# Performance work log

Hardware: AMD Instinct MI355X
Metric: run time of the kernel (lower is better)

The kernel has to match this reference:

```python
import jax, jax.numpy as jnp
import numpy as np

S, I = 512, 384
C_MSA, C_Z, H, C = 64, 128, 8, 32
EPS = 1e-5


def _layernorm(x, g, b):
    mu = jnp.mean(x, axis=-1, keepdims=True)
    var = jnp.var(x, axis=-1, keepdims=True)
    return (x - mu) * jax.lax.rsqrt(var + EPS) * g + b


def setup_inputs() -> dict:
    key = jax.random.key(0)
    ks = jax.random.split(key, 6)
    sc_v = 1.0 / np.sqrt(C_MSA)
    sc_z = 1.0 / np.sqrt(C_Z)
    sc_o = 1.0 / np.sqrt(H * C)
    return {
        "msa_SI": jax.random.normal(ks[0], (S, I, C_MSA), jnp.float32),
        "pair_II": jax.random.normal(ks[1], (I, I, C_Z), jnp.float32),
        "ln_msa_g": jnp.ones((C_MSA,), jnp.float32),
        "ln_msa_b": jnp.zeros((C_MSA,), jnp.float32),
        "ln_pair_g": jnp.ones((C_Z,), jnp.float32),
        "ln_pair_b": jnp.zeros((C_Z,), jnp.float32),
        "W_v": jax.random.normal(ks[2], (C_MSA, H * C), jnp.float32) * sc_v,
        "W_bias": jax.random.normal(ks[3], (C_Z, H), jnp.float32) * sc_z,
        "W_gate": jax.random.normal(ks[4], (C_MSA, H * C), jnp.float32) * sc_v,
        "W_out": jax.random.normal(ks[5], (H * C, C_MSA), jnp.float32) * sc_o,
    }


def reference(msa_SI, pair_II, ln_msa_g, ln_msa_b, ln_pair_g, ln_pair_b,
              W_v, W_bias, W_gate, W_out):
    s, i = msa_SI.shape[:2]
    msa_n = _layernorm(msa_SI, ln_msa_g, ln_msa_b)              # [S,I,Cm]
    v_SIHC = (msa_n @ W_v).reshape(s, i, H, C)                   # [S,I,H,C]
    bias_IIH = _layernorm(pair_II, ln_pair_g, ln_pair_b) @ W_bias  # [I,I,H]
    w_IIH = jax.nn.softmax(bias_IIH, axis=-2)                    # softmax over j
    gate = jax.nn.sigmoid(msa_n @ W_gate)                        # [S,I,H*C]
    # weighted average shared across S: [I,I,H] x [S,I,H,C] -> [S,I,H,C]
    weights = jnp.einsum('ijh,sjhc->sihc', w_IIH, v_SIHC).reshape(s, i, H * C)
    o = gate * weights
    return o @ W_out                                             # [S,I,Cm]
```

## Files before the change

### kernel.cpp

```cpp
#include <hip/hip_runtime.h>
#include <hip/hip_bf16.h>

#define S_DIM 512
#define I_DIM 384
#define CM 64
#define CZ 128
#define H_DIM 8
#define C_DIM 32
#define HC 256
#define II (I_DIM*I_DIM)

typedef short bf16x8 __attribute__((ext_vector_type(8)));
typedef float f32x4 __attribute__((ext_vector_type(4)));

__device__ __forceinline__ float s2f(short s) {
    unsigned int u = ((unsigned int)(unsigned short)s) << 16;
    float f; __builtin_memcpy(&f, &u, 4); return f;
}
__device__ __forceinline__ short f2bf(float f) {
    __hip_bfloat16 h = __float2bfloat16(f);
    short r; __builtin_memcpy(&r, &h, 2); return r;
}

__device__ __forceinline__ void glds16(const short* g, short* l) {
    __builtin_amdgcn_global_load_lds(
        (const __attribute__((address_space(1))) void*)g,
        (__attribute__((address_space(3))) void*)l, 16, 0, 0);
}

__global__ __launch_bounds__(256) void k_pair_ln_bias(
    const float* __restrict__ pair, const float* __restrict__ g,
    const float* __restrict__ b, const float* __restrict__ Wb,
    float* __restrict__ bias)
{
    __shared__ float xs[4][CZ];
    __shared__ float WbT[H_DIM*132];
    const int tid = threadIdx.x;
    const int wv = tid >> 6, lane = tid & 63;
    const int ij = blockIdx.x*4 + wv;

    {
        float4 q = *(const float4*)(Wb + tid*4);
        int m = tid*4;
        WbT[(m&7)*132 + (m>>3)]     = q.x;
        WbT[((m+1)&7)*132 + ((m+1)>>3)] = q.y;
        WbT[((m+2)&7)*132 + ((m+2)>>3)] = q.z;
        WbT[((m+3)&7)*132 + ((m+3)>>3)] = q.w;
    }

    float2 x2 = *(const float2*)(pair + (size_t)ij*CZ + lane*2);
    float s1 = x2.x + x2.y;
    float s2 = x2.x*x2.x + x2.y*x2.y;
#pragma unroll
    for (int off = 32; off > 0; off >>= 1) {
        s1 += __shfl_xor(s1, off, 64);
        s2 += __shfl_xor(s2, off, 64);
    }
    float mu = s1 * (1.f/CZ);
    float var = s2 * (1.f/CZ) - mu*mu;
    float rs = rsqrtf(var + 1e-5f);
    xs[wv][lane*2]   = (x2.x - mu)*rs*g[lane*2]   + b[lane*2];
    xs[wv][lane*2+1] = (x2.y - mu)*rs*g[lane*2+1] + b[lane*2+1];
    __syncthreads();

    const int h = lane >> 3, seg = lane & 7;
    float p = 0.f;
#pragma unroll
    for (int jj = 0; jj < 16; jj++) {
        int c = seg + jj*8;
        p += xs[wv][c] * WbT[h*132 + c];
    }
    p += __shfl_down(p, 4, 64);
    p += __shfl_down(p, 2, 64);
    p += __shfl_down(p, 1, 64);
    if (seg == 0) bias[(size_t)h*II + ij] = p;
}

__global__ __launch_bounds__(384) void k_softmax(
    const float* __restrict__ bias, short* __restrict__ w)
{
    int blk = blockIdx.x;
    int i = blk >> 3, h = blk & 7;
    int j = threadIdx.x;
    float x = bias[(size_t)h*II + i*I_DIM + j];
    float m = x;
#pragma unroll
    for (int off = 32; off > 0; off >>= 1) m = fmaxf(m, __shfl_xor(m, off, 64));
    __shared__ float red[6];
    int wv = j >> 6;
    if ((j & 63) == 0) red[wv] = m;
    __syncthreads();
    m = red[0];
#pragma unroll
    for (int k = 1; k < 6; k++) m = fmaxf(m, red[k]);
    float e = __expf(x - m);
    float s = e;
#pragma unroll
    for (int off = 32; off > 0; off >>= 1) s += __shfl_xor(s, off, 64);
    __syncthreads();
    if ((j & 63) == 0) red[wv] = s;
    __syncthreads();
    s = 0.f;
#pragma unroll
    for (int k = 0; k < 6; k++) s += red[k];
    w[(size_t)h*II + i*I_DIM + j] = f2bf(e / s);
}

__global__ __launch_bounds__(256) void k_prep_w(
    const float* __restrict__ Wv, const float* __restrict__ Wg,
    const float* __restrict__ Wo,
    short* __restrict__ Wt, short* __restrict__ Wot)
{
    int idx = blockIdx.x*256 + threadIdx.x;
    if (idx < 512*64) {
        int n = idx >> 6, k = idx & 63;
        Wt[idx] = f2bf((n < HC) ? Wv[k*HC + n] : Wg[k*HC + (n - HC)]);
    } else {
        int q = idx - 512*64;
        int n = q >> 8, k = q & 255;
        Wot[q] = f2bf(Wo[k*64 + n]);
    }
}

__global__ __launch_bounds__(256) void k4_ln_vgate(
    const float* __restrict__ msa_c,
    const float* __restrict__ gm, const float* __restrict__ bm,
    const short* __restrict__ Wt,
    short* __restrict__ v_t, short* __restrict__ gate)
{
    __shared__ alignas(16) short lds[20992];
    short* As = lds;
    short* Bs = lds + 4608;
    short* T  = lds;

    const int tid = threadIdx.x;
    const int wave = tid >> 6;
    const int lane = tid & 63;
    const int pm = blockIdx.y;

    {
        const int row = tid >> 2;
        const int seg = tid & 3;
        float xf[16], gf[16], bf[16];
        const float* rp = msa_c + (size_t)(pm*64 + row)*CM + seg*16;
#pragma unroll
        for (int q = 0; q < 4; q++) {
            float4 a = *(const float4*)(rp + q*4);
            xf[q*4] = a.x; xf[q*4+1] = a.y; xf[q*4+2] = a.z; xf[q*4+3] = a.w;
            float4 gg = *(const float4*)(gm + seg*16 + q*4);
            gf[q*4] = gg.x; gf[q*4+1] = gg.y; gf[q*4+2] = gg.z; gf[q*4+3] = gg.w;
            float4 bb = *(const float4*)(bm + seg*16 + q*4);
            bf[q*4] = bb.x; bf[q*4+1] = bb.y; bf[q*4+2] = bb.z; bf[q*4+3] = bb.w;
        }
        float s1 = 0.f, s2 = 0.f;
#pragma unroll
        for (int j = 0; j < 16; j++) { s1 += xf[j]; s2 += xf[j]*xf[j]; }
        s1 += __shfl_xor(s1, 1); s2 += __shfl_xor(s2, 1);
        s1 += __shfl_xor(s1, 2); s2 += __shfl_xor(s2, 2);
        float mu = s1 * (1.f/64.f);
        float var = s2 * (1.f/64.f) - mu*mu;
        float rs = rsqrtf(var + 1e-5f);
        bf16x8 o0, o1;
#pragma unroll
        for (int j = 0; j < 8; j++) {
            o0[j] = f2bf((xf[j]   - mu)*rs*gf[j]   + bf[j]);
            o1[j] = f2bf((xf[8+j] - mu)*rs*gf[8+j] + bf[8+j]);
        }
        *(bf16x8*)&As[row*72 + seg*16]     = o0;
        *(bf16x8*)&As[row*72 + seg*16 + 8] = o1;
    }

    const int lr = lane >> 2, lq = lane & 3;
    const int fr = lane & 15, fq = lane >> 4;
    f32x4 acc[4][8] = {};

    for (int kt = 0; kt < 2; ++kt) {
#pragma unroll
        for (int c2 = 0; c2 < 8; c2++) {
            int ch = wave + c2*4;
            glds16(Wt + (ch*16 + lr)*64 + kt*32 + lq*8, &Bs[ch*512]);
        }
        __syncthreads();

        bf16x8 af[4], bfrag[8];
#pragma unroll
        for (int mi = 0; mi < 4; mi++)
            af[mi] = *(const bf16x8*)&As[(mi*16 + fr)*72 + kt*32 + fq*8];
#pragma unroll
        for (int ni = 0; ni < 8; ni++)
            bfrag[ni] = *(const bf16x8*)&Bs[(wave*128 + ni*16 + fr)*32 + fq*8];
#pragma unroll
        for (int mi = 0; mi < 4; mi++)
#pragma unroll
            for (int ni = 0; ni < 8; ni++)
                acc[mi][ni] = __builtin_amdgcn_mfma_f32_16x16x32_bf16(
                    af[mi], bfrag[ni], acc[mi][ni], 0, 0, 0);
        __syncthreads();
    }

    const int s_local = pm / 6;
    const int j0 = (pm % 6) * 64;
    if (wave < 2) {
#pragma unroll
        for (int mi = 0; mi < 4; mi++)
#pragma unroll
        for (int ni = 0; ni < 8; ni++) {
            int cl = wave*128 + ni*16 + fr;
            short4 pk;
            pk.x = f2bf(acc[mi][ni][0]);
            pk.y = f2bf(acc[mi][ni][1]);
            pk.z = f2bf(acc[mi][ni][2]);
            pk.w = f2bf(acc[mi][ni][3]);
            *(short4*)&T[cl*72 + mi*16 + fq*4] = pk;
        }
    } else {
#pragma unroll
        for (int mi = 0; mi < 4; mi++)
#pragma unroll
        for (int ni = 0; ni < 8; ni++)
#pragma unroll
        for (int r = 0; r < 4; r++) {
            int rowg = pm*64 + mi*16 + fq*4 + r;
            int col = (wave - 2)*128 + ni*16 + fr;
            gate[(size_t)rowg*HC + col] =
                f2bf(1.f/(1.f + __expf(-acc[mi][ni][r])));
        }
    }
    __syncthreads();
#pragma unroll
    for (int p = 0; p < 8; p++) {
        int unit = p*256 + tid;
        int cl = unit >> 3, part = unit & 7;
        bf16x8 d = *(const bf16x8*)&T[cl*72 + part*8];
        int h = cl >> 5, cc = cl & 31;
        *(bf16x8*)&v_t[(((size_t)s_local*H_DIM + h)*C_DIM + cc)*I_DIM + j0 + part*8] = d;
    }
}

__global__ __launch_bounds__(512, 2) void k56_einsum_proj(
    const short* __restrict__ w,
    const short* __restrict__ v_t,
    const short* __restrict__ gate,
    const short* __restrict__ Wot,
    float* __restrict__ out)
{
    __shared__ alignas(16) short Ws[3][192*32];
    __shared__ alignas(16) short Ob[8][32*40];
    const int tid = threadIdx.x;
    const int wave = tid >> 6, lane = tid & 63;
    const int fr = lane & 15, fq = lane >> 4;
    const int ibase = blockIdx.x * 192;
    const int sg = blockIdx.y;
    const int ms = wave >> 1;
    const int kv = wave & 1;
    const int s  = sg*4 + ms;
    const int iw = kv * 96;

    const short* vts = v_t + (size_t)s * H_DIM * C_DIM * I_DIM;

    auto stage = [&](int h_, int kt_, int buf) {
        const short* base = w + (size_t)h_*II + (size_t)kt_*32;
        {
            int row = wave*16 + (lane >> 2);
            int q = (lane & 3) ^ ((row >> 1) & 3);
            glds16(base + (size_t)(ibase + row)*I_DIM + q*8,
                   &Ws[buf][wave*16*32]);
        }
        if (wave < 4) {
            int row = (8 + wave)*16 + (lane >> 2);
            int q = (lane & 3) ^ ((row >> 1) & 3);
            glds16(base + (size_t)(ibase + row)*I_DIM + q*8,
                   &Ws[buf][(8 + wave)*16*32]);
        }
    };
    auto loadAv = [&](bf16x8* d, int h_, int kt_) {
        const short* vb = vts + (size_t)h_*(C_DIM*I_DIM) + kt_*32;
        d[0] = *(const bf16x8*)&vb[fr*I_DIM + fq*8];
        d[1] = *(const bf16x8*)&vb[(16 + fr)*I_DIM + fq*8];
    };

    f32x4 acc_o[6][4] = {};
    bf16x8 avs[3][2];

    loadAv(avs[0], 0, 0);
    loadAv(avs[1], 0, 1);
    __builtin_amdgcn_sched_barrier(0);
    stage(0, 0, 0);
    stage(0, 1, 1);
    stage(0, 2, 2);
    __builtin_amdgcn_sched_barrier(0);

#pragma unroll 1
    for (int h = 0; h < H_DIM; h++) {
        f32x4 acc_e[2][6] = {};
#pragma unroll
        for (int kt = 0; kt < 12; kt++) {
            const int cb = kt % 3;
            if (h == 0 && kt == 0) {
                if (wave < 4) asm volatile("s_waitcnt vmcnt(4)" ::: "memory");
                else          asm volatile("s_waitcnt vmcnt(2)" ::: "memory");
            } else if (h == 7 && kt == 10) {
                if (wave < 4) asm volatile("s_waitcnt vmcnt(4)" ::: "memory");
                else          asm volatile("s_waitcnt vmcnt(3)" ::: "memory");
            } else if (h == 7 && kt == 11) {
                asm volatile("s_waitcnt vmcnt(0)" ::: "memory");
            } else {
                if (wave < 4) asm volatile("s_waitcnt vmcnt(6)" ::: "memory");
                else          asm volatile("s_waitcnt vmcnt(4)" ::: "memory");
            }
            __builtin_amdgcn_s_barrier();
            __builtin_amdgcn_sched_barrier(0);

            bf16x8 bwv[6];
#pragma unroll
            for (int ni = 0; ni < 6; ni++) {
                int row = iw + ni*16 + fr;
                bwv[ni] = *(const bf16x8*)
                    &Ws[cb][row*32 + ((fq ^ ((row >> 1) & 3)) << 3)];
            }
            if (kt < 10)      loadAv(avs[(kt+2)%3], h, kt + 2);
            else if (h < 7)   loadAv(avs[(kt+2)%3], h + 1, kt - 10);
            __builtin_amdgcn_sched_barrier(0);

            asm volatile("s_waitcnt lgkmcnt(0)" ::: "memory");
            __builtin_amdgcn_sched_barrier(0);
            __builtin_amdgcn_s_barrier();
            __builtin_amdgcn_sched_barrier(0);

            if (kt < 9)       stage(h, kt + 3, cb);
            else if (h < 7)   stage(h + 1, kt - 9, cb);
            __builtin_amdgcn_sched_barrier(0);

            __builtin_amdgcn_s_setprio(1);
#pragma unroll
            for (int mi = 0; mi < 2; mi++)
#pragma unroll
                for (int ni = 0; ni < 6; ni++)
                    acc_e[mi][ni] = __builtin_amdgcn_mfma_f32_16x16x32_bf16(
                        avs[cb][mi], bwv[ni], acc_e[mi][ni], 0, 0, 0);
            __builtin_amdgcn_s_setprio(0);
        }

        bf16x8 bw[4];
#pragma unroll
        for (int ni = 0; ni < 4; ni++)
            bw[ni] = *(const bf16x8*)&Wot[(ni*16 + fr)*HC + h*C_DIM + fq*8];
        short4 gv[2][6];
#pragma unroll
        for (int mi = 0; mi < 2; mi++)
#pragma unroll
        for (int ni = 0; ni < 6; ni++)
            gv[mi][ni] = *(const short4*)&gate[
                (size_t)(s*I_DIM + ibase + iw + ni*16 + fr)*HC
                + h*C_DIM + mi*16 + fq*4];

        short* myOb = Ob[wave];
#pragma unroll
        for (int p = 0; p < 3; p++) {
#pragma unroll
            for (int t = 0; t < 2; t++) {
                int ni = p*2 + t;
#pragma unroll
                for (int mi = 0; mi < 2; mi++) {
                    short4 g = gv[mi][ni];
                    short4 pk;
                    pk.x = f2bf(acc_e[mi][ni][0] * s2f(g.x));
                    pk.y = f2bf(acc_e[mi][ni][1] * s2f(g.y));
                    pk.z = f2bf(acc_e[mi][ni][2] * s2f(g.z));
                    pk.w = f2bf(acc_e[mi][ni][3] * s2f(g.w));
                    *(short4*)&myOb[(t*16 + fr)*40 + mi*16 + fq*4] = pk;
                }
            }
            bf16x8 ao[2];
#pragma unroll
            for (int t = 0; t < 2; t++)
                ao[t] = *(const bf16x8*)&myOb[(t*16 + fr)*40 + fq*8];
            __builtin_amdgcn_s_setprio(1);
#pragma unroll
            for (int t = 0; t < 2; t++)
#pragma unroll
                for (int ni = 0; ni < 4; ni++)
                    acc_o[p*2 + t][ni] = __builtin_amdgcn_mfma_f32_16x16x32_bf16(
                        ao[t], bw[ni], acc_o[p*2 + t][ni], 0, 0, 0);
            __builtin_amdgcn_s_setprio(0);
        }
    }

#pragma unroll
    for (int mi = 0; mi < 6; mi++)
#pragma unroll
    for (int ni = 0; ni < 4; ni++)
#pragma unroll
    for (int r = 0; r < 4; r++) {
        int i = ibase + iw + mi*16 + fq*4 + r;
        int n = ni*16 + fr;
        out[(size_t)(s*I_DIM + i)*CM + n] = acc_o[mi][ni][r];
    }
}

extern "C" void kernel_launch(void* const* d_in, const int* in_sizes, int n_in,
                              void* d_out, int out_size, void* d_ws, size_t ws_size,
                              hipStream_t stream)
{
    const float* msa  = (const float*)d_in[0];
    const float* pair = (const float*)d_in[1];
    const float* gm   = (const float*)d_in[2];
    const float* bm   = (const float*)d_in[3];
    const float* gp   = (const float*)d_in[4];
    const float* bp   = (const float*)d_in[5];
    const float* Wv   = (const float*)d_in[6];
    const float* Wb   = (const float*)d_in[7];
    const float* Wg   = (const float*)d_in[8];
    const float* Wo   = (const float*)d_in[9];

    char* ws = (char*)d_ws;
    short* w    = (short*)ws;
    short* Wt   = (short*)(ws + 2359296);
    short* Wot  = (short*)(ws + 2424832);
    char*  region = ws + 2457600;
    float* bias = (float*)region;

    size_t avail = (ws_size > 2457600u) ? (ws_size - 2457600u) : 0;
    int Sc = 8;
    const int scs[7] = {512, 256, 128, 64, 32, 16, 8};
    for (int i = 0; i < 7; i++) {
        size_t need = (size_t)scs[i] * 393216u;
        if (need < 4718592u) need = 4718592u;
        if (need <= avail) { Sc = scs[i]; break; }
    }
    const int NC = S_DIM / Sc;
    short* v_t  = (short*)region;
    short* gate = (short*)(region + (size_t)Sc*196608u);

    k_pair_ln_bias<<<dim3(II/4), dim3(256), 0, stream>>>(pair, gp, bp, Wb, bias);
    k_prep_w<<<dim3(192), dim3(256), 0, stream>>>(Wv, Wg, Wo, Wt, Wot);
    k_softmax<<<dim3(I_DIM*H_DIM), dim3(I_DIM), 0, stream>>>(bias, w);

    for (int c = 0; c < NC; c++) {
        size_t in_off = (size_t)c * Sc * I_DIM * CM;

        k4_ln_vgate<<<dim3(1, Sc*6, 1), dim3(256), 0, stream>>>(
            msa + in_off, gm, bm, Wt, v_t, gate);

        k56_einsum_proj<<<dim3(2, Sc/4), dim3(512), 0, stream>>>(
            w, v_t, gate, Wot, (float*)d_out + in_off);
    }
}
```

Baseline: 411.2 us.

## Tile w and v_t into 32-wide k-blocks, coalesce gate stores, prefetch epilogue loads

The softmax weights and transposed V are stored in k-tile-blocked layouts (32 contiguous j per row block), so the einsum kernel's LDS staging and A-operand loads read contiguous 1–2 KB chunks. The gate sigmoid output is staged through shared memory and written with 16-byte coalesced stores instead of scattered 2-byte writes. The W_out and gate loads for each head's epilogue are issued two k-steps early, inside the MFMA loop, with the vmcnt waits adjusted so their latency overlaps compute. This relies on hand-tuned waitcnt counts being exactly right and adds extra syncthreads to the projection kernel.

```diff
diff --git a/kernel.cpp b/kernel.cpp
--- a/kernel.cpp
+++ b/kernel.cpp
@@ -103,7 +103,7 @@
     s = 0.f;
 #pragma unroll
     for (int k = 0; k < 6; k++) s += red[k];
-    w[(size_t)h*II + i*I_DIM + j] = f2bf(e / s);
+    w[(((size_t)h*12 + (j>>5))*I_DIM + i)*32 + (j&31)] = f2bf(e / s);
 }
 
 __global__ __launch_bounds__(256) void k_prep_w(
@@ -213,18 +213,6 @@
             pk.w = f2bf(acc[mi][ni][3]);
             *(short4*)&T[cl*72 + mi*16 + fq*4] = pk;
         }
-    } else {
-#pragma unroll
-        for (int mi = 0; mi < 4; mi++)
-#pragma unroll
-        for (int ni = 0; ni < 8; ni++)
-#pragma unroll
-        for (int r = 0; r < 4; r++) {
-            int rowg = pm*64 + mi*16 + fq*4 + r;
-            int col = (wave - 2)*128 + ni*16 + fr;
-            gate[(size_t)rowg*HC + col] =
-                f2bf(1.f/(1.f + __expf(-acc[mi][ni][r])));
-        }
     }
     __syncthreads();
 #pragma unroll
@@ -233,7 +221,30 @@
         int cl = unit >> 3, part = unit & 7;
         bf16x8 d = *(const bf16x8*)&T[cl*72 + part*8];
         int h = cl >> 5, cc = cl & 31;
-        *(bf16x8*)&v_t[(((size_t)s_local*H_DIM + h)*C_DIM + cc)*I_DIM + j0 + part*8] = d;
+        int ktb = (j0 >> 5) + (part >> 2);
+        *(bf16x8*)&v_t[(((size_t)s_local*H_DIM + h)*12 + ktb)*1024
+                       + cc*32 + (part&3)*8] = d;
+    }
+    __syncthreads();
+    if (wave >= 2) {
+#pragma unroll
+        for (int mi = 0; mi < 4; mi++)
+#pragma unroll
+        for (int ni = 0; ni < 8; ni++)
+#pragma unroll
+        for (int r = 0; r < 4; r++) {
+            int row = mi*16 + fq*4 + r;
+            int col = (wave - 2)*128 + ni*16 + fr;
+            T[row*264 + col] = f2bf(1.f/(1.f + __expf(-acc[mi][ni][r])));
+        }
+    }
+    __syncthreads();
+#pragma unroll
+    for (int p = 0; p < 8; p++) {
+        int unit = p*256 + tid;
+        int row = unit >> 5, ch = unit & 31;
+        bf16x8 d = *(const bf16x8*)&T[row*264 + ch*8];
+        *(bf16x8*)&gate[(size_t)(pm*64 + row)*HC + ch*8] = d;
     }
 }
 
@@ -256,27 +267,21 @@
     const int s  = sg*4 + ms;
     const int iw = kv * 96;
 
-    const short* vts = v_t + (size_t)s * H_DIM * C_DIM * I_DIM;
+    const short* vts = v_t + (size_t)s * (H_DIM*12*1024);
 
     auto stage = [&](int h_, int kt_, int buf) {
-        const short* base = w + (size_t)h_*II + (size_t)kt_*32;
-        {
-            int row = wave*16 + (lane >> 2);
-            int q = (lane & 3) ^ ((row >> 1) & 3);
-            glds16(base + (size_t)(ibase + row)*I_DIM + q*8,
-                   &Ws[buf][wave*16*32]);
-        }
-        if (wave < 4) {
-            int row = (8 + wave)*16 + (lane >> 2);
-            int q = (lane & 3) ^ ((row >> 1) & 3);
-            glds16(base + (size_t)(ibase + row)*I_DIM + q*8,
+        const short* base = w + (((size_t)h_*12 + kt_)*I_DIM + ibase)*32;
+        const int r4 = lane >> 2;
+        const int q  = (lane & 3) ^ ((lane >> 3) & 3);
+        glds16(base + (wave*16 + r4)*32 + q*8, &Ws[buf][wave*16*32]);
+        if (wave < 4)
+            glds16(base + ((8 + wave)*16 + r4)*32 + q*8,
                    &Ws[buf][(8 + wave)*16*32]);
-        }
     };
     auto loadAv = [&](bf16x8* d, int h_, int kt_) {
-        const short* vb = vts + (size_t)h_*(C_DIM*I_DIM) + kt_*32;
-        d[0] = *(const bf16x8*)&vb[fr*I_DIM + fq*8];
-        d[1] = *(const bf16x8*)&vb[(16 + fr)*I_DIM + fq*8];
+        const short* vb = vts + ((size_t)h_*12 + kt_)*1024;
+        d[0] = *(const bf16x8*)&vb[fr*32 + fq*8];
+        d[1] = *(const bf16x8*)&vb[(16 + fr)*32 + fq*8];
     };
 
     f32x4 acc_o[6][4] = {};
@@ -293,17 +298,24 @@
 #pragma unroll 1
     for (int h = 0; h < H_DIM; h++) {
         f32x4 acc_e[2][6] = {};
+        short4 gv[2][6];
+        bf16x8 bw[4];
 #pragma unroll
         for (int kt = 0; kt < 12; kt++) {
             const int cb = kt % 3;
             if (h == 0 && kt == 0) {
                 if (wave < 4) asm volatile("s_waitcnt vmcnt(4)" ::: "memory");
                 else          asm volatile("s_waitcnt vmcnt(2)" ::: "memory");
+            } else if (kt == 11) {
+                if (h < 7) {
+                    if (wave < 4) asm volatile("s_waitcnt vmcnt(22)" ::: "memory");
+                    else          asm volatile("s_waitcnt vmcnt(20)" ::: "memory");
+                } else {
+                    asm volatile("s_waitcnt vmcnt(16)" ::: "memory");
+                }
             } else if (h == 7 && kt == 10) {
                 if (wave < 4) asm volatile("s_waitcnt vmcnt(4)" ::: "memory");
                 else          asm volatile("s_waitcnt vmcnt(3)" ::: "memory");
-            } else if (h == 7 && kt == 11) {
-                asm volatile("s_waitcnt vmcnt(0)" ::: "memory");
             } else {
                 if (wave < 4) asm volatile("s_waitcnt vmcnt(6)" ::: "memory");
                 else          asm volatile("s_waitcnt vmcnt(4)" ::: "memory");
@@ -331,6 +343,20 @@
             else if (h < 7)   stage(h + 1, kt - 9, cb);
             __builtin_amdgcn_sched_barrier(0);
 
+            if (kt == 10) {
+#pragma unroll
+                for (int ni = 0; ni < 4; ni++)
+                    bw[ni] = *(const bf16x8*)&Wot[(ni*16 + fr)*HC + h*C_DIM + fq*8];
+#pragma unroll
+                for (int mi = 0; mi < 2; mi++)
+#pragma unroll
+                for (int ni = 0; ni < 6; ni++)
+                    gv[mi][ni] = *(const short4*)&gate[
+                        (size_t)(s*I_DIM + ibase + iw + ni*16 + fr)*HC
+                        + h*C_DIM + mi*16 + fq*4];
+                __builtin_amdgcn_sched_barrier(0);
+            }
+
             __builtin_amdgcn_s_setprio(1);
 #pragma unroll
             for (int mi = 0; mi < 2; mi++)
@@ -340,19 +366,6 @@
                         avs[cb][mi], bwv[ni], acc_e[mi][ni], 0, 0, 0);
             __builtin_amdgcn_s_setprio(0);
         }
-
-        bf16x8 bw[4];
-#pragma unroll
-        for (int ni = 0; ni < 4; ni++)
-            bw[ni] = *(const bf16x8*)&Wot[(ni*16 + fr)*HC + h*C_DIM + fq*8];
-        short4 gv[2][6];
-#pragma unroll
-        for (int mi = 0; mi < 2; mi++)
-#pragma unroll
-        for (int ni = 0; ni < 6; ni++)
-            gv[mi][ni] = *(const short4*)&gate[
-                (size_t)(s*I_DIM + ibase + iw + ni*16 + fr)*HC
-                + h*C_DIM + mi*16 + fq*4];
 
         short* myOb = Ob[wave];
 #pragma unroll
```

Result: slower. 437.9 us (+6.5%).

## Stage V tiles through LDS, coalesce gate stores, prefetch gate early, remap blocks

Applied to the files above, without the earlier changes.

The einsum kernel now loads V tiles into shared memory with async global-to-LDS copies, alongside the W tiles, in a double-buffered pipeline. Previously each wave did its own direct global register loads from a triple-buffered scheme. The gate and Wot loads are issued at kt==10, so they overlap the last MFMA steps instead of stalling after the loop. The LN/vgate kernel now stages sigmoid gate values in LDS and writes them with coalesced 16-byte stores instead of scattered 2-byte stores. The grid becomes 1D with a swizzled block-to-(s,i) mapping, presumably to improve cache locality. Dropping to two buffers reduces prefetch depth, which may expose memory latency.

```diff
diff --git a/kernel.cpp b/kernel.cpp
--- a/kernel.cpp
+++ b/kernel.cpp
@@ -213,18 +213,6 @@
             pk.w = f2bf(acc[mi][ni][3]);
             *(short4*)&T[cl*72 + mi*16 + fq*4] = pk;
         }
-    } else {
-#pragma unroll
-        for (int mi = 0; mi < 4; mi++)
-#pragma unroll
-        for (int ni = 0; ni < 8; ni++)
-#pragma unroll
-        for (int r = 0; r < 4; r++) {
-            int rowg = pm*64 + mi*16 + fq*4 + r;
-            int col = (wave - 2)*128 + ni*16 + fr;
-            gate[(size_t)rowg*HC + col] =
-                f2bf(1.f/(1.f + __expf(-acc[mi][ni][r])));
-        }
     }
     __syncthreads();
 #pragma unroll
@@ -235,6 +223,27 @@
         int h = cl >> 5, cc = cl & 31;
         *(bf16x8*)&v_t[(((size_t)s_local*H_DIM + h)*C_DIM + cc)*I_DIM + j0 + part*8] = d;
     }
+    __syncthreads();
+    if (wave >= 2) {
+#pragma unroll
+        for (int mi = 0; mi < 4; mi++)
+#pragma unroll
+        for (int ni = 0; ni < 8; ni++)
+#pragma unroll
+        for (int r = 0; r < 4; r++) {
+            int row = mi*16 + fq*4 + r;
+            int col = (wave - 2)*128 + ni*16 + fr;
+            T[row*264 + col] = f2bf(1.f/(1.f + __expf(-acc[mi][ni][r])));
+        }
+    }
+    __syncthreads();
+#pragma unroll
+    for (int p = 0; p < 8; p++) {
+        int unit = p*256 + tid;
+        int row = unit >> 5, ch = unit & 31;
+        bf16x8 d = *(const bf16x8*)&T[row*264 + ch*8];
+        *(bf16x8*)&gate[(size_t)(pm*64 + row)*HC + ch*8] = d;
+    }
 }
 
 __global__ __launch_bounds__(512, 2) void k56_einsum_proj(
@@ -244,91 +253,102 @@
     const short* __restrict__ Wot,
     float* __restrict__ out)
 {
-    __shared__ alignas(16) short Ws[3][192*32];
+    __shared__ alignas(16) short Ws[2][192*32];
+    __shared__ alignas(16) short Vs[2][4][1024];
     __shared__ alignas(16) short Ob[8][32*40];
     const int tid = threadIdx.x;
     const int wave = tid >> 6, lane = tid & 63;
     const int fr = lane & 15, fq = lane >> 4;
-    const int ibase = blockIdx.x * 192;
-    const int sg = blockIdx.y;
+
+    int bb = blockIdx.x;
+    int ih, sg;
+    if ((gridDim.x & 15) == 0) {
+        int nb16 = gridDim.x >> 4;
+        sg = (bb & 7)*nb16 + ((bb >> 3) >> 1);
+        ih = (bb >> 3) & 1;
+    } else { ih = bb & 1; sg = bb >> 1; }
+
+    const int ibase = ih * 192;
     const int ms = wave >> 1;
     const int kv = wave & 1;
     const int s  = sg*4 + ms;
     const int iw = kv * 96;
 
-    const short* vts = v_t + (size_t)s * H_DIM * C_DIM * I_DIM;
+    const int vs_s = wave >> 1;
+    const int vs_h = wave & 1;
+    const short* vstage = v_t + ((size_t)(sg*4 + vs_s)*H_DIM)*(C_DIM*I_DIM);
 
     auto stage = [&](int h_, int kt_, int buf) {
         const short* base = w + (size_t)h_*II + (size_t)kt_*32;
         {
             int row = wave*16 + (lane >> 2);
             int q = (lane & 3) ^ ((row >> 1) & 3);
-            glds16(base + (size_t)(ibase + row)*I_DIM + q*8,
-                   &Ws[buf][wave*16*32]);
+            glds16(base + (size_t)(ibase + row)*I_DIM + q*8, &Ws[buf][wave*512]);
         }
         if (wave < 4) {
             int row = (8 + wave)*16 + (lane >> 2);
             int q = (lane & 3) ^ ((row >> 1) & 3);
-            glds16(base + (size_t)(ibase + row)*I_DIM + q*8,
-                   &Ws[buf][(8 + wave)*16*32]);
+            glds16(base + (size_t)(ibase + row)*I_DIM + q*8, &Ws[buf][(8+wave)*512]);
+        }
+        {
+            int c = vs_h*16 + (lane >> 2);
+            int q = (lane & 3) ^ ((c >> 1) & 3);
+            glds16(vstage + (size_t)h_*(C_DIM*I_DIM) + (size_t)c*I_DIM + kt_*32 + q*8,
+                   &Vs[buf][vs_s][vs_h*512]);
         }
     };
-    auto loadAv = [&](bf16x8* d, int h_, int kt_) {
-        const short* vb = vts + (size_t)h_*(C_DIM*I_DIM) + kt_*32;
-        d[0] = *(const bf16x8*)&vb[fr*I_DIM + fq*8];
-        d[1] = *(const bf16x8*)&vb[(16 + fr)*I_DIM + fq*8];
-    };
 
     f32x4 acc_o[6][4] = {};
-    bf16x8 avs[3][2];
-
-    loadAv(avs[0], 0, 0);
-    loadAv(avs[1], 0, 1);
-    __builtin_amdgcn_sched_barrier(0);
+
     stage(0, 0, 0);
     stage(0, 1, 1);
-    stage(0, 2, 2);
-    __builtin_amdgcn_sched_barrier(0);
 
 #pragma unroll 1
     for (int h = 0; h < H_DIM; h++) {
         f32x4 acc_e[2][6] = {};
+        short4 gv[2][6];
+        bf16x8 bw[4];
 #pragma unroll
         for (int kt = 0; kt < 12; kt++) {
-            const int cb = kt % 3;
-            if (h == 0 && kt == 0) {
-                if (wave < 4) asm volatile("s_waitcnt vmcnt(4)" ::: "memory");
-                else          asm volatile("s_waitcnt vmcnt(2)" ::: "memory");
-            } else if (h == 7 && kt == 10) {
-                if (wave < 4) asm volatile("s_waitcnt vmcnt(4)" ::: "memory");
-                else          asm volatile("s_waitcnt vmcnt(3)" ::: "memory");
-            } else if (h == 7 && kt == 11) {
-                asm volatile("s_waitcnt vmcnt(0)" ::: "memory");
-            } else {
-                if (wave < 4) asm volatile("s_waitcnt vmcnt(6)" ::: "memory");
-                else          asm volatile("s_waitcnt vmcnt(4)" ::: "memory");
-            }
+            const int cb = kt & 1;
+            if (wave < 4) asm volatile("s_waitcnt vmcnt(3)" ::: "memory");
+            else          asm volatile("s_waitcnt vmcnt(2)" ::: "memory");
             __builtin_amdgcn_s_barrier();
             __builtin_amdgcn_sched_barrier(0);
 
-            bf16x8 bwv[6];
+            bf16x8 av[2], bwv[6];
+#pragma unroll
+            for (int mi = 0; mi < 2; mi++) {
+                int row = mi*16 + fr;
+                av[mi] = *(const bf16x8*)
+                    &Vs[cb][ms][row*32 + ((fq ^ ((row >> 1) & 3)) << 3)];
+            }
 #pragma unroll
             for (int ni = 0; ni < 6; ni++) {
                 int row = iw + ni*16 + fr;
                 bwv[ni] = *(const bf16x8*)
                     &Ws[cb][row*32 + ((fq ^ ((row >> 1) & 3)) << 3)];
             }
-            if (kt < 10)      loadAv(avs[(kt+2)%3], h, kt + 2);
-            else if (h < 7)   loadAv(avs[(kt+2)%3], h + 1, kt - 10);
-            __builtin_amdgcn_sched_barrier(0);
-
             asm volatile("s_waitcnt lgkmcnt(0)" ::: "memory");
             __builtin_amdgcn_sched_barrier(0);
             __builtin_amdgcn_s_barrier();
             __builtin_amdgcn_sched_barrier(0);
 
-            if (kt < 9)       stage(h, kt + 3, cb);
-            else if (h < 7)   stage(h + 1, kt - 9, cb);
+            if (kt == 10) {
+#pragma unroll
+                for (int ni = 0; ni < 4; ni++)
+                    bw[ni] = *(const bf16x8*)&Wot[(ni*16 + fr)*HC + h*C_DIM + fq*8];
+#pragma unroll
+                for (int mi = 0; mi < 2; mi++)
+#pragma unroll
+                for (int ni = 0; ni < 6; ni++)
+                    gv[mi][ni] = *(const short4*)&gate[
+                        (size_t)(s*I_DIM + ibase + iw + ni*16 + fr)*HC
+                        + h*C_DIM + mi*16 + fq*4];
+                __builtin_amdgcn_sched_barrier(0);
+            }
+            if (kt < 10)      stage(h, kt + 2, cb);
+            else if (h < 7)   stage(h + 1, kt - 10, cb);
             __builtin_amdgcn_sched_barrier(0);
 
             __builtin_amdgcn_s_setprio(1);
@@ -337,22 +357,9 @@
 #pragma unroll
                 for (int ni = 0; ni < 6; ni++)
                     acc_e[mi][ni] = __builtin_amdgcn_mfma_f32_16x16x32_bf16(
-                        avs[cb][mi], bwv[ni], acc_e[mi][ni], 0, 0, 0);
+                        av[mi], bwv[ni], acc_e[mi][ni], 0, 0, 0);
             __builtin_amdgcn_s_setprio(0);
         }
-
-        bf16x8 bw[4];
-#pragma unroll
-        for (int ni = 0; ni < 4; ni++)
-            bw[ni] = *(const bf16x8*)&Wot[(ni*16 + fr)*HC + h*C_DIM + fq*8];
-        short4 gv[2][6];
-#pragma unroll
-        for (int mi = 0; mi < 2; mi++)
-#pragma unroll
-        for (int ni = 0; ni < 6; ni++)
-            gv[mi][ni] = *(const short4*)&gate[
-                (size_t)(s*I_DIM + ibase + iw + ni*16 + fr)*HC
-                + h*C_DIM + mi*16 + fq*4];
 
         short* myOb = Ob[wave];
 #pragma unroll
@@ -442,7 +449,7 @@
         k4_ln_vgate<<<dim3(1, Sc*6, 1), dim3(256), 0, stream>>>(
             msa + in_off, gm, bm, Wt, v_t, gate);
 
-        k56_einsum_proj<<<dim3(2, Sc/4), dim3(512), 0, stream>>>(
+        k56_einsum_proj<<<dim3(Sc/2), dim3(512), 0, stream>>>(
             w, v_t, gate, Wot, (float*)d_out + in_off);
     }
 }
```

Result: no change. 412.2 us (+0.2%).
